# Kernel optimization log

Measured on AMD Instinct MI355X. Metric: run time of the kernel, lower is better.

The kernel has to match this reference:

```python
import jax, jax.numpy as jnp
import numpy as np

N = 10000   # num_nodes (batch=1)
E = 160000  # num edges
CIN, H, T, OUT, K = 32, 64, 12, 12, 3


def _conv1d(x, w, b, pad):
    # x: [N, C_in, T], w: [C_out, C_in, K]
    out = jax.lax.conv_general_dilated(
        x, w, window_strides=(1,), padding=[(pad, pad)],
        dimension_numbers=('NCH', 'OIH', 'NCH'))
    return out + b[None, :, None]


def _gated_tconv(x, w, b):
    # GatedTemporalConv (dropout = identity in eval)
    out = _conv1d(x, w, b, K // 2)
    P, Q = jnp.split(out, 2, axis=1)
    return P * jax.nn.sigmoid(Q)


def _gcn(x, W, b, src, dst, ew):
    # PyG GCNConv, vectorized over all T timesteps in one fused pass.
    # x: [N, C_in, T], W: [C_out, C_in]
    xt = jnp.einsum('nct,oc->not', x, W)
    loop = jnp.arange(N)
    srcl = jnp.concatenate([src, loop])
    dstl = jnp.concatenate([dst, loop])
    ewl = jnp.concatenate([ew, jnp.ones((N,), ew.dtype)])
    deg = jax.ops.segment_sum(ewl, dstl, num_segments=N)
    dis = jnp.where(deg > 0, jax.lax.rsqrt(deg), 0.0)
    norm = dis[srcl] * ewl * dis[dstl]                      # [E+N]
    msg = xt[srcl] * norm[:, None, None]                    # [E+N, C_out, T]
    out = jax.ops.segment_sum(msg, dstl, num_segments=N)    # [N, C_out, T]
    return out + b[None, :, None]


def setup_inputs() -> dict:
    key = jax.random.key(0)
    ks = jax.random.split(key, 20)
    rn = lambda k, s: jax.random.normal(k, s, jnp.float32) * 0.05
    return {
        'x': jax.random.normal(ks[0], (N, CIN, T), jnp.float32),
        'edge_index': jax.random.randint(ks[1], (2, E), 0, N),
        'edge_weight': jax.random.uniform(ks[2], (E,), jnp.float32),
        'tc1a_w': rn(ks[3], (2 * H, CIN, K)), 'tc1a_b': rn(ks[4], (2 * H,)),
        'gc1_w': rn(ks[5], (H, H)),           'gc1_b': rn(ks[6], (H,)),
        'tc1b_w': rn(ks[7], (2 * H, H, K)),   'tc1b_b': rn(ks[8], (2 * H,)),
        'tc2a_w': rn(ks[9], (2 * H, H, K)),   'tc2a_b': rn(ks[10], (2 * H,)),
        'gc2_w': rn(ks[11], (H, H)),          'gc2_b': rn(ks[12], (H,)),
        'tc2b_w': rn(ks[13], (2 * H, H, K)),  'tc2b_b': rn(ks[14], (2 * H,)),
        'fin_w': rn(ks[15], (OUT, H, T)),     'fin_b': rn(ks[16], (OUT,)),
    }


def reference(x, edge_index, edge_weight,
              tc1a_w, tc1a_b, gc1_w, gc1_b, tc1b_w, tc1b_b,
              tc2a_w, tc2a_b, gc2_w, gc2_b, tc2b_w, tc2b_b,
              fin_w, fin_b):
    src, dst = edge_index[0], edge_index[1]
    h = _gated_tconv(x, tc1a_w, tc1a_b)
    h = jax.nn.relu(_gcn(h, gc1_w, gc1_b, src, dst, edge_weight))
    h = _gated_tconv(h, tc1b_w, tc1b_b)
    h = _gated_tconv(h, tc2a_w, tc2a_b)
    h = jax.nn.relu(_gcn(h, gc2_w, gc2_b, src, dst, edge_weight))
    h = _gated_tconv(h, tc2b_w, tc2b_b)
    h = _conv1d(h, fin_w, fin_b, 0)          # [N, OUT, 1] (kernel == T)
    h = h[:, :, 0]                            # squeeze(-1)
    return h.reshape(1, N, OUT)               # batch_size = 1
```

## Files before the change

### kernel.cpp

```cpp
#include <hip/hip_runtime.h>
#include <hip/hip_bf16.h>
#include <stdint.h>

#define N_NODES 10000
#define N_EDGES 160000
#define BUCKET 128

typedef unsigned short u16;
typedef unsigned int u32;
typedef short s16v8 __attribute__((ext_vector_type(8)));
typedef float f32v4 __attribute__((ext_vector_type(4)));

__device__ __forceinline__ float bf2f(u16 v){ return __uint_as_float(((u32)v) << 16); }
__device__ __forceinline__ u16 f2bf(float f){
    u32 u = __float_as_uint(f);
    u32 r = (u + 0x7fffu + ((u >> 16) & 1u)) >> 16;
    return (u16)r;
}

struct SmallPtrs { const void* p[14]; };

__device__ __constant__ const int g_seg_off[15] = {
    0, 12288, 12416, 16512, 16576, 41152, 41280,
    65856, 65984, 70080, 70144, 94720, 94848, 104064, 104076
};
__device__ __constant__ const int g_seg_kind[14] = {
    1, 0, 0, 0, 2, 0, 2, 0, 0, 0, 2, 0, 0, 0
};

__global__ void k_convert_init(SmallPtrs ps, u16* __restrict__ dst,
                               float* deg, int* cur){
    int i = blockIdx.x * blockDim.x + threadIdx.x;
    if (i < 104076){
        int seg = 0, base = 0;
#pragma unroll
        for (int s = 0; s < 14; s++){
            if (i >= g_seg_off[s]){ seg = s; base = g_seg_off[s]; }
        }
        int li = i - base;
        float v = ((const float*)ps.p[seg])[li];
        int kind = g_seg_kind[seg];
        int dsto = li;
        if (kind){
            int CIN = (kind == 1) ? 32 : 64;
            int o = li / (3 * CIN);
            int rem = li - o * (3 * CIN);
            int c = rem / 3, d = rem - c * 3;
            dsto = d * 128 * CIN + o * CIN + c;
        }
        dst[base + dsto] = f2bf(v);
    }
    if (i < N_NODES){ deg[i] = 1.0f; cur[i] = 0; }
}

__launch_bounds__(256, 4)
__global__ void k_gconv_count(const float* __restrict__ xin, const u16* __restrict__ wg,
                              const u16* __restrict__ bg, u16* __restrict__ out,
                              const int* __restrict__ ei, const float* __restrict__ ew,
                              float* deg, int* cur, int2* __restrict__ epack){
    if (blockIdx.x >= 1250){
        int e = (blockIdx.x - 1250) * 256 + threadIdx.x;
        if (e < N_EDGES){
            int s = ei[e];
            int d = ei[N_EDGES + e];
            float wv = ew[e];
            atomicAdd(&deg[d], wv);
            int p = atomicAdd(&cur[d], 1);
            if (p < BUCKET) epack[d * BUCKET + p] = make_int2(s, __float_as_int(wv));
        }
        return;
    }
    __shared__ __attribute__((aligned(16))) u16 shbuf[6912];
    u16* xT = shbuf;
    u16* Ho = shbuf;
    int tid = threadIdx.x;
    int n0 = blockIdx.x * 8;

    int lane = tid & 63, wave = tid >> 6;
    int col = lane & 15, quad = lane >> 4;
    int o_p = wave * 16 + col, o_q = o_p + 64;

    s16v8 Bf[3][2];
#pragma unroll
    for (int pq = 0; pq < 2; pq++){
        int o = pq ? o_q : o_p;
#pragma unroll
        for (int d = 0; d < 3; d++)
            Bf[d][pq] = *(const s16v8*)(wg + d * 4096 + o * 32 + quad * 8);
    }

    for (int i = tid; i < 8 * 40; i += 256){
        int g = i / 40, c = i % 40;
        xT[g * 560 + 0 * 40 + c] = 0; xT[g * 560 + 13 * 40 + c] = 0;
    }
    {
        int g = tid >> 5, c = tid & 31;
        const float4* p = (const float4*)(xin + ((size_t)(n0 + g) * 32 + c) * 12);
        float4 v0 = p[0], v1 = p[1], v2 = p[2];
        u16* xb = xT + g * 560 + c;
        xb[1 * 40] = f2bf(v0.x);  xb[2 * 40] = f2bf(v0.y);
        xb[3 * 40] = f2bf(v0.z);  xb[4 * 40] = f2bf(v0.w);
        xb[5 * 40] = f2bf(v1.x);  xb[6 * 40] = f2bf(v1.y);
        xb[7 * 40] = f2bf(v1.z);  xb[8 * 40] = f2bf(v1.w);
        xb[9 * 40] = f2bf(v2.x);  xb[10 * 40] = f2bf(v2.y);
        xb[11 * 40] = f2bf(v2.z); xb[12 * 40] = f2bf(v2.w);
    }
    __syncthreads();

    f32v4 aP[6], aQ[6];
#pragma unroll
    for (int mt = 0; mt < 6; mt++){ aP[mt] = (f32v4)0.f; aQ[mt] = (f32v4)0.f; }
#pragma unroll
    for (int mt = 0; mt < 6; mt++){
        int m = mt * 16 + col;
        int g = m / 12, t = m - 12 * g;
#pragma unroll
        for (int d = 0; d < 3; d++){
            s16v8 a = *(const s16v8*)&xT[g * 560 + (t + d) * 40 + quad * 8];
            aP[mt] = __builtin_amdgcn_mfma_f32_16x16x32_bf16(a, Bf[d][0], aP[mt], 0, 0, 0);
            aQ[mt] = __builtin_amdgcn_mfma_f32_16x16x32_bf16(a, Bf[d][1], aQ[mt], 0, 0, 0);
        }
    }
    __syncthreads();
    float bP = bf2f(bg[o_p]), bQ = bf2f(bg[o_q]);
#pragma unroll
    for (int mt = 0; mt < 6; mt++){
#pragma unroll
        for (int r = 0; r < 4; r++){
            int m2 = mt * 16 + quad * 4 + r;
            int g = m2 / 12, t = m2 - 12 * g;
            float pv = aP[mt][r] + bP, qv = aQ[mt][r] + bQ;
            Ho[g * 864 + t * 72 + o_p] = f2bf(pv / (1.f + __expf(-qv)));
        }
    }
    __syncthreads();
    for (int i = tid; i < 768; i += 256){
        int g = i / 96, r = i % 96, t = r / 8, ch = r % 8;
        *(s16v8*)(out + (size_t)(n0 + g) * 768 + t * 64 + ch * 8) =
            *(const s16v8*)&Ho[g * 864 + t * 72 + ch * 8];
    }
}

__global__ void k_norm(const float* __restrict__ deg, const int* __restrict__ cur,
                       int2* __restrict__ ep){
    int i = blockIdx.x * blockDim.x + threadIdx.x;
    int n = i >> 7, slot = i & 127;
    if (n >= N_NODES) return;
    int cnt = cur[n]; if (cnt > BUCKET) cnt = BUCKET;
    if (slot < cnt){
        int2 e = ep[(size_t)n * BUCKET + slot];
        float w = __int_as_float(e.y) * rsqrtf(deg[e.x]) * rsqrtf(deg[n]);
        ep[(size_t)n * BUCKET + slot].y = __float_as_int(w);
    }
}

__launch_bounds__(256, 4)
__global__ void k_gather(const u16* __restrict__ src, const float* __restrict__ deg,
                         const int* __restrict__ cur, const int2* __restrict__ ep,
                         u16* __restrict__ z){
    int slice = blockIdx.x & 7;
    int nb = blockIdx.x >> 3;
    int tid = threadIdx.x;
    int nl = tid >> 5;
    int sub = tid & 31;
    int eg = sub >> 3;
    int l8 = sub & 7;
    int n = nb * 8 + nl;
    int base = slice * 96 + l8 * 12;

    float acc[12];
    if (eg == 0){
        float sw = 1.0f / deg[n];
        const u16* xr = src + (size_t)n * 768 + base;
#pragma unroll
        for (int k = 0; k < 3; k++){
            ushort4 v = *(const ushort4*)(xr + k * 4);
            acc[k * 4 + 0] = sw * bf2f(v.x); acc[k * 4 + 1] = sw * bf2f(v.y);
            acc[k * 4 + 2] = sw * bf2f(v.z); acc[k * 4 + 3] = sw * bf2f(v.w);
        }
    } else {
#pragma unroll
        for (int k = 0; k < 12; k++) acc[k] = 0.f;
    }

    int e = cur[n]; if (e > BUCKET) e = BUCKET;
    const int2* eb = ep + (size_t)n * BUCKET;
    int p = eg;
    for (; p + 4 < e; p += 8){
        int2 e0 = eb[p], e1 = eb[p + 4];
        float w0 = __int_as_float(e0.y), w1 = __int_as_float(e1.y);
        const u16* q0 = src + (size_t)e0.x * 768 + base;
        const u16* q1 = src + (size_t)e1.x * 768 + base;
        ushort4 a0 = *(const ushort4*)(q0);
        ushort4 a1 = *(const ushort4*)(q0 + 4);
        ushort4 a2 = *(const ushort4*)(q0 + 8);
        ushort4 c0 = *(const ushort4*)(q1);
        ushort4 c1 = *(const ushort4*)(q1 + 4);
        ushort4 c2 = *(const ushort4*)(q1 + 8);
        acc[0] = fmaf(w0, bf2f(a0.x), acc[0]); acc[1] = fmaf(w0, bf2f(a0.y), acc[1]);
        acc[2] = fmaf(w0, bf2f(a0.z), acc[2]); acc[3] = fmaf(w0, bf2f(a0.w), acc[3]);
        acc[4] = fmaf(w0, bf2f(a1.x), acc[4]); acc[5] = fmaf(w0, bf2f(a1.y), acc[5]);
        acc[6] = fmaf(w0, bf2f(a1.z), acc[6]); acc[7] = fmaf(w0, bf2f(a1.w), acc[7]);
        acc[8] = fmaf(w0, bf2f(a2.x), acc[8]); acc[9] = fmaf(w0, bf2f(a2.y), acc[9]);
        acc[10] = fmaf(w0, bf2f(a2.z), acc[10]); acc[11] = fmaf(w0, bf2f(a2.w), acc[11]);
        acc[0] = fmaf(w1, bf2f(c0.x), acc[0]); acc[1] = fmaf(w1, bf2f(c0.y), acc[1]);
        acc[2] = fmaf(w1, bf2f(c0.z), acc[2]); acc[3] = fmaf(w1, bf2f(c0.w), acc[3]);
        acc[4] = fmaf(w1, bf2f(c1.x), acc[4]); acc[5] = fmaf(w1, bf2f(c1.y), acc[5]);
        acc[6] = fmaf(w1, bf2f(c1.z), acc[6]); acc[7] = fmaf(w1, bf2f(c1.w), acc[7]);
        acc[8] = fmaf(w1, bf2f(c2.x), acc[8]); acc[9] = fmaf(w1, bf2f(c2.y), acc[9]);
        acc[10] = fmaf(w1, bf2f(c2.z), acc[10]); acc[11] = fmaf(w1, bf2f(c2.w), acc[11]);
    }
    if (p < e){
        int2 e0 = eb[p];
        float w0 = __int_as_float(e0.y);
        const u16* q0 = src + (size_t)e0.x * 768 + base;
#pragma unroll
        for (int k = 0; k < 3; k++){
            ushort4 v = *(const ushort4*)(q0 + k * 4);
            acc[k * 4 + 0] = fmaf(w0, bf2f(v.x), acc[k * 4 + 0]);
            acc[k * 4 + 1] = fmaf(w0, bf2f(v.y), acc[k * 4 + 1]);
            acc[k * 4 + 2] = fmaf(w0, bf2f(v.z), acc[k * 4 + 2]);
            acc[k * 4 + 3] = fmaf(w0, bf2f(v.w), acc[k * 4 + 3]);
        }
    }
#pragma unroll
    for (int k = 0; k < 12; k++){
        acc[k] += __shfl_xor(acc[k], 8, 64);
        acc[k] += __shfl_xor(acc[k], 16, 64);
    }
    if (eg == 0){
        u16* zo = z + (size_t)n * 768 + base;
#pragma unroll
        for (int k = 0; k < 3; k++){
            ushort4 hv;
            hv.x = f2bf(acc[k * 4 + 0]); hv.y = f2bf(acc[k * 4 + 1]);
            hv.z = f2bf(acc[k * 4 + 2]); hv.w = f2bf(acc[k * 4 + 3]);
            *(ushort4*)(zo + k * 4) = hv;
        }
    }
}

#define XIDX(g, row, c) (((g) * 14 + (row)) * 72 + (c))

template<bool LAST>
__launch_bounds__(256, 4)
__global__ void k_fused(const u16* __restrict__ z,
                        const u16* __restrict__ Wmix, const u16* __restrict__ bmix,
                        const u16* __restrict__ w1, const u16* __restrict__ b1,
                        const u16* __restrict__ w2, const u16* __restrict__ b2,
                        const u16* __restrict__ fw, const u16* __restrict__ fb,
                        u16* __restrict__ outMid, float* __restrict__ outFin){
    __shared__ __attribute__((aligned(16))) u16 bufX[8 * 14 * 72];
    __shared__ __attribute__((aligned(16))) u16 bufY[8 * 14 * 72];
    int tid = threadIdx.x;
    int n0 = blockIdx.x * 8;
    int lane = tid & 63, wave = tid >> 6;
    int col = lane & 15, quad = lane >> 4;
    int o_p = wave * 16 + col, o_q = o_p + 64;

    for (int i = tid; i < 8 * 72; i += 256){
        int g = i / 72, c = i % 72;
        bufX[XIDX(g, 0, c)] = 0; bufX[XIDX(g, 13, c)] = 0;
        bufY[XIDX(g, 0, c)] = 0; bufY[XIDX(g, 13, c)] = 0;
    }
    for (int i = tid; i < 768; i += 256){
        int g = i / 96, r = i % 96, t = r >> 3, ch = r & 7;
        *(s16v8*)&bufX[XIDX(g, 1 + t, ch * 8)] =
            *(const s16v8*)(z + (size_t)(n0 + g) * 768 + t * 64 + ch * 8);
    }
    __syncthreads();

    {
        f32v4 accm[6];
#pragma unroll
        for (int mt = 0; mt < 6; mt++) accm[mt] = (f32v4)0.f;
#pragma unroll
        for (int ks = 0; ks < 2; ks++){
            s16v8 Bm = *(const s16v8*)(Wmix + (size_t)o_p * 64 + ks * 32 + quad * 8);
#pragma unroll
            for (int mt = 0; mt < 6; mt++){
                int m = mt * 16 + col;
                int g = m / 12, t = m - 12 * g;
                s16v8 a = *(const s16v8*)&bufX[XIDX(g, 1 + t, ks * 32 + quad * 8)];
                accm[mt] = __builtin_amdgcn_mfma_f32_16x16x32_bf16(a, Bm, accm[mt], 0, 0, 0);
            }
        }
        float bm = bf2f(bmix[o_p]);
#pragma unroll
        for (int mt = 0; mt < 6; mt++){
#pragma unroll
            for (int r = 0; r < 4; r++){
                int m2 = mt * 16 + quad * 4 + r;
                int g = m2 / 12, t = m2 - 12 * g;
                bufY[XIDX(g, 1 + t, o_p)] = f2bf(fmaxf(accm[mt][r] + bm, 0.f));
            }
        }
    }
    __syncthreads();

    {
        f32v4 aP[6], aQ[6];
#pragma unroll
        for (int mt = 0; mt < 6; mt++){ aP[mt] = (f32v4)0.f; aQ[mt] = (f32v4)0.f; }
#pragma unroll
        for (int ks = 0; ks < 2; ks++){
            s16v8 Bf[3][2];
#pragma unroll
            for (int pq = 0; pq < 2; pq++){
                int o = pq ? o_q : o_p;
#pragma unroll
                for (int d = 0; d < 3; d++)
                    Bf[d][pq] = *(const s16v8*)(w1 + d * 8192 + o * 64 + ks * 32 + quad * 8);
            }
#pragma unroll
            for (int mt = 0; mt < 6; mt++){
                int m = mt * 16 + col;
                int g = m / 12, t = m - 12 * g;
#pragma unroll
                for (int d = 0; d < 3; d++){
                    s16v8 a = *(const s16v8*)&bufY[XIDX(g, t + d, ks * 32 + quad * 8)];
                    aP[mt] = __builtin_amdgcn_mfma_f32_16x16x32_bf16(a, Bf[d][0], aP[mt], 0, 0, 0);
                    aQ[mt] = __builtin_amdgcn_mfma_f32_16x16x32_bf16(a, Bf[d][1], aQ[mt], 0, 0, 0);
                }
            }
        }
        float bP = bf2f(b1[o_p]), bQ = bf2f(b1[o_q]);
#pragma unroll
        for (int mt = 0; mt < 6; mt++){
#pragma unroll
            for (int r = 0; r < 4; r++){
                int m2 = mt * 16 + quad * 4 + r;
                int g = m2 / 12, t = m2 - 12 * g;
                float pv = aP[mt][r] + bP, qv = aQ[mt][r] + bQ;
                u16 hv = f2bf(pv / (1.f + __expf(-qv)));
                if (LAST) bufX[g * 1008 + o_p * 12 + t] = hv;
                else      bufX[XIDX(g, 1 + t, o_p)] = hv;
            }
        }
    }
    __syncthreads();

    if (!LAST){
        f32v4 aP[6], aQ[6];
#pragma unroll
        for (int mt = 0; mt < 6; mt++){ aP[mt] = (f32v4)0.f; aQ[mt] = (f32v4)0.f; }
#pragma unroll
        for (int ks = 0; ks < 2; ks++){
            s16v8 Bf[3][2];
#pragma unroll
            for (int pq = 0; pq < 2; pq++){
                int o = pq ? o_q : o_p;
#pragma unroll
                for (int d = 0; d < 3; d++)
                    Bf[d][pq] = *(const s16v8*)(w2 + d * 8192 + o * 64 + ks * 32 + quad * 8);
            }
#pragma unroll
            for (int mt = 0; mt < 6; mt++){
                int m = mt * 16 + col;
                int g = m / 12, t = m - 12 * g;
#pragma unroll
                for (int d = 0; d < 3; d++){
                    s16v8 a = *(const s16v8*)&bufX[XIDX(g, t + d, ks * 32 + quad * 8)];
                    aP[mt] = __builtin_amdgcn_mfma_f32_16x16x32_bf16(a, Bf[d][0], aP[mt], 0, 0, 0);
                    aQ[mt] = __builtin_amdgcn_mfma_f32_16x16x32_bf16(a, Bf[d][1], aQ[mt], 0, 0, 0);
                }
            }
        }
        float bP = bf2f(b2[o_p]), bQ = bf2f(b2[o_q]);
#pragma unroll
        for (int mt = 0; mt < 6; mt++){
#pragma unroll
            for (int r = 0; r < 4; r++){
                int m2 = mt * 16 + quad * 4 + r;
                int g = m2 / 12, t = m2 - 12 * g;
                float pv = aP[mt][r] + bP, qv = aQ[mt][r] + bQ;
                bufY[XIDX(g, 1 + t, o_p)] = f2bf(pv / (1.f + __expf(-qv)));
            }
        }
        __syncthreads();
        for (int i = tid; i < 768; i += 256){
            int g = i / 96, r = i % 96, t = r / 8, ch = r % 8;
            *(s16v8*)(outMid + (size_t)(n0 + g) * 768 + t * 64 + ch * 8) =
                *(const s16v8*)&bufY[XIDX(g, 1 + t, ch * 8)];
        }
    } else {
        if (wave == 0){
            f32v4 accF = {0.f, 0.f, 0.f, 0.f};
            int g8 = col & 7;
#pragma unroll
            for (int ks = 0; ks < 24; ks++){
                s16v8 a = *(const s16v8*)&bufX[g8 * 1008 + ks * 32 + quad * 8];
                s16v8 bfr = {0, 0, 0, 0, 0, 0, 0, 0};
                if (col < 12)
                    bfr = *(const s16v8*)(fw + (size_t)col * 768 + ks * 32 + quad * 8);
                accF = __builtin_amdgcn_mfma_f32_16x16x32_bf16(a, bfr, accF, 0, 0, 0);
            }
            if (col < 12 && quad < 2){
                float bb = bf2f(fb[col]);
#pragma unroll
                for (int r = 0; r < 4; r++){
                    int g = quad * 4 + r;
                    outFin[(size_t)(n0 + g) * 12 + col] = accF[r] + bb;
                }
            }
        }
    }
}

static inline size_t align256(size_t x){ return (x + 255) & ~(size_t)255; }

extern "C" void kernel_launch(void* const* d_in, const int* in_sizes, int n_in,
                              void* d_out, int out_size, void* d_ws, size_t ws_size,
                              hipStream_t stream){
    const float* x  = (const float*)d_in[0];
    const int* ei   = (const int*)d_in[1];
    const float* ew = (const float*)d_in[2];

    char* w = (char*)d_ws;
    u16* bufA    = (u16*)w;  w += align256((size_t)N_NODES * 768 * sizeof(u16));
    u16* bufB    = (u16*)w;  w += align256((size_t)N_NODES * 768 * sizeof(u16));
    u16* zA      = (u16*)w;  w += align256((size_t)N_NODES * 768 * sizeof(u16));
    u16* zB      = (u16*)w;  w += align256((size_t)N_NODES * 768 * sizeof(u16));
    float* deg   = (float*)w; w += align256(N_NODES * sizeof(float));
    int* cur     = (int*)w;   w += align256(N_NODES * sizeof(int));
    int2* epack  = (int2*)w;  w += align256((size_t)N_NODES * BUCKET * sizeof(int2));
    u16* cvt     = (u16*)w;   w += align256(104076 * sizeof(u16));

    u16* tc1a_w = cvt + 0;
    u16* tc1a_b = cvt + 12288;
    u16* gc1_w  = cvt + 12416;
    u16* gc1_b  = cvt + 16512;
    u16* tc1b_w = cvt + 16576;
    u16* tc1b_b = cvt + 41152;
    u16* tc2a_w = cvt + 41280;
    u16* tc2a_b = cvt + 65856;
    u16* gc2_w  = cvt + 65984;
    u16* gc2_b  = cvt + 70080;
    u16* tc2b_w = cvt + 70144;
    u16* tc2b_b = cvt + 94720;
    u16* fin_w  = cvt + 94848;
    u16* fin_b  = cvt + 104064;

    SmallPtrs ps;
    ps.p[0]  = d_in[3];  ps.p[1]  = d_in[4];
    ps.p[2]  = d_in[5];  ps.p[3]  = d_in[6];
    ps.p[4]  = d_in[7];  ps.p[5]  = d_in[8];
    ps.p[6]  = d_in[9];  ps.p[7]  = d_in[10];
    ps.p[8]  = d_in[11]; ps.p[9]  = d_in[12];
    ps.p[10] = d_in[13]; ps.p[11] = d_in[14];
    ps.p[12] = d_in[15]; ps.p[13] = d_in[16];

    k_convert_init<<<(104076 + 255) / 256, 256, 0, stream>>>(ps, cvt, deg, cur);
    k_gconv_count<<<1250 + 625, 256, 0, stream>>>(x, tc1a_w, tc1a_b, bufA, ei, ew, deg, cur, epack);
    k_norm<<<(N_NODES * BUCKET) / 256, 256, 0, stream>>>(deg, cur, epack);

    k_gather<<<1250 * 8, 256, 0, stream>>>(bufA, deg, cur, epack, zA);
    k_fused<false><<<1250, 256, 0, stream>>>(zA, gc1_w, gc1_b, tc1b_w, tc1b_b,
                                             tc2a_w, tc2a_b, nullptr, nullptr,
                                             bufB, nullptr);
    k_gather<<<1250 * 8, 256, 0, stream>>>(bufB, deg, cur, epack, zB);
    k_fused<true><<<1250, 256, 0, stream>>>(zB, gc2_w, gc2_b, tc2b_w, tc2b_b,
                                            nullptr, nullptr, fin_w, fin_b,
                                            nullptr, (float*)d_out);
}
```

Measured before the change: 232.1 us.

## Widen gather to a full wave per node and reorder edge-count blocks first

The gather kernel now assigns 64 lanes per node (8 edge groups instead of 4) in 512-thread blocks and loads two packed edge entries with one int4 read, adding a third shuffle reduction step. The combined conv/count kernel places edge-counting blocks first so the atomics start early, and the input load is rewritten for coalesced float4 reads across the node tile. The aim is more memory-level parallelism for the irregular neighbour gathers and better-coalesced input loads, at the cost of idle lanes for low-degree nodes and an extra reduction stage.

```diff
diff --git a/kernel.cpp b/kernel.cpp
--- a/kernel.cpp
+++ b/kernel.cpp
@@ -58,8 +58,8 @@
                               const u16* __restrict__ bg, u16* __restrict__ out,
                               const int* __restrict__ ei, const float* __restrict__ ew,
                               float* deg, int* cur, int2* __restrict__ epack){
-    if (blockIdx.x >= 1250){
-        int e = (blockIdx.x - 1250) * 256 + threadIdx.x;
+    if (blockIdx.x < 625){
+        int e = blockIdx.x * 256 + threadIdx.x;
         if (e < N_EDGES){
             int s = ei[e];
             int d = ei[N_EDGES + e];
@@ -74,7 +74,7 @@
     u16* xT = shbuf;
     u16* Ho = shbuf;
     int tid = threadIdx.x;
-    int n0 = blockIdx.x * 8;
+    int n0 = (blockIdx.x - 625) * 8;
 
     int lane = tid & 63, wave = tid >> 6;
     int col = lane & 15, quad = lane >> 4;
@@ -94,16 +94,19 @@
         xT[g * 560 + 0 * 40 + c] = 0; xT[g * 560 + 13 * 40 + c] = 0;
     }
     {
-        int g = tid >> 5, c = tid & 31;
-        const float4* p = (const float4*)(xin + ((size_t)(n0 + g) * 32 + c) * 12);
-        float4 v0 = p[0], v1 = p[1], v2 = p[2];
-        u16* xb = xT + g * 560 + c;
-        xb[1 * 40] = f2bf(v0.x);  xb[2 * 40] = f2bf(v0.y);
-        xb[3 * 40] = f2bf(v0.z);  xb[4 * 40] = f2bf(v0.w);
-        xb[5 * 40] = f2bf(v1.x);  xb[6 * 40] = f2bf(v1.y);
-        xb[7 * 40] = f2bf(v1.z);  xb[8 * 40] = f2bf(v1.w);
-        xb[9 * 40] = f2bf(v2.x);  xb[10 * 40] = f2bf(v2.y);
-        xb[11 * 40] = f2bf(v2.z); xb[12 * 40] = f2bf(v2.w);
+        const float* xb = xin + (size_t)n0 * 384;
+#pragma unroll
+        for (int it = 0; it < 3; it++){
+            int f = it * 1024 + tid * 4;
+            float4 v = *(const float4*)(xb + f);
+            int g = f / 384, rem = f - g * 384;
+            int c = rem / 12, t = rem - c * 12;
+            u16* dst = xT + g * 560 + (1 + t) * 40 + c;
+            dst[0 * 40] = f2bf(v.x);
+            dst[1 * 40] = f2bf(v.y);
+            dst[2 * 40] = f2bf(v.z);
+            dst[3 * 40] = f2bf(v.w);
+        }
     }
     __syncthreads();
 
@@ -154,17 +157,17 @@
     }
 }
 
-__launch_bounds__(256, 4)
-__global__ void k_gather(const u16* __restrict__ src, const float* __restrict__ deg,
-                         const int* __restrict__ cur, const int2* __restrict__ ep,
+__launch_bounds__(512, 4)
+__global__ void k_gather(const u16* __restrict__ src, const int* __restrict__ cur,
+                         const int2* __restrict__ ep, const float* __restrict__ deg,
                          u16* __restrict__ z){
     int slice = blockIdx.x & 7;
     int nb = blockIdx.x >> 3;
     int tid = threadIdx.x;
-    int nl = tid >> 5;
-    int sub = tid & 31;
-    int eg = sub >> 3;
-    int l8 = sub & 7;
+    int nl = tid >> 6;
+    int lane = tid & 63;
+    int eg = lane >> 3;
+    int l8 = lane & 7;
     int n = nb * 8 + nl;
     int base = slice * 96 + l8 * 12;
 
@@ -185,12 +188,12 @@
 
     int e = cur[n]; if (e > BUCKET) e = BUCKET;
     const int2* eb = ep + (size_t)n * BUCKET;
-    int p = eg;
-    for (; p + 4 < e; p += 8){
-        int2 e0 = eb[p], e1 = eb[p + 4];
-        float w0 = __int_as_float(e0.y), w1 = __int_as_float(e1.y);
-        const u16* q0 = src + (size_t)e0.x * 768 + base;
-        const u16* q1 = src + (size_t)e1.x * 768 + base;
+    int p = eg * 2;
+    for (; p + 1 < e; p += 16){
+        int4 epr = *(const int4*)&eb[p];
+        float w0 = __int_as_float(epr.y), w1 = __int_as_float(epr.w);
+        const u16* q0 = src + (size_t)epr.x * 768 + base;
+        const u16* q1 = src + (size_t)epr.z * 768 + base;
         ushort4 a0 = *(const ushort4*)(q0);
         ushort4 a1 = *(const ushort4*)(q0 + 4);
         ushort4 a2 = *(const ushort4*)(q0 + 8);
@@ -227,6 +230,7 @@
     for (int k = 0; k < 12; k++){
         acc[k] += __shfl_xor(acc[k], 8, 64);
         acc[k] += __shfl_xor(acc[k], 16, 64);
+        acc[k] += __shfl_xor(acc[k], 32, 64);
     }
     if (eg == 0){
         u16* zo = z + (size_t)n * 768 + base;
@@ -454,11 +458,11 @@
     k_gconv_count<<<1250 + 625, 256, 0, stream>>>(x, tc1a_w, tc1a_b, bufA, ei, ew, deg, cur, epack);
     k_norm<<<(N_NODES * BUCKET) / 256, 256, 0, stream>>>(deg, cur, epack);
 
-    k_gather<<<1250 * 8, 256, 0, stream>>>(bufA, deg, cur, epack, zA);
+    k_gather<<<1250 * 8, 512, 0, stream>>>(bufA, cur, epack, deg, zA);
     k_fused<false><<<1250, 256, 0, stream>>>(zA, gc1_w, gc1_b, tc1b_w, tc1b_b,
                                              tc2a_w, tc2a_b, nullptr, nullptr,
                                              bufB, nullptr);
-    k_gather<<<1250 * 8, 256, 0, stream>>>(bufB, deg, cur, epack, zB);
+    k_gather<<<1250 * 8, 512, 0, stream>>>(bufB, cur, epack, deg, zB);
     k_fused<true><<<1250, 256, 0, stream>>>(zB, gc2_w, gc2_b, tc2b_w, tc2b_b,
                                             nullptr, nullptr, fin_w, fin_b,
                                             nullptr, (float*)d_out);
```

After: 264.4 us. 1.14x slower.
